# Kernel tuning notes

Hardware: AMD Instinct MI355X
Metric: run time of the kernel (lower is better)

Reference implementation:

```python
import jax, jax.numpy as jnp
import numpy as np


def squash(s, axis=-1):
    sq = jnp.sum(jnp.square(s), axis=axis, keepdims=True)
    scale = sq / (1.0 + sq) / (jnp.sqrt(sq) + 1e-08)
    return scale * s


def setup_inputs() -> dict:
    key = jax.random.key(0)
    k1, k2 = jax.random.split(key)
    # [B, input_num_caps, input_dim_caps]
    x = jax.random.normal(k1, (64, 1152, 8), dtype=jnp.float32)
    # W: [input_num_caps, num_capsules, input_dim_caps, dim_capsules]
    W = jax.random.normal(k2, (1152, 32, 8, 16), dtype=jnp.float32) * 0.05
    return {"x": x, "W": W}


def reference(x, W):
    # Original tiles x along the output-capsule axis before the einsum
    # 'bicd,icde->bice'; since the tiled copies are identical along c,
    # this is exactly 'bid,icde->bice' without materializing the tile.
    u_hat = jnp.einsum('bid,icde->bice', x, W)  # [B, I, C, E]
    b = jnp.zeros(u_hat.shape[:3], dtype=u_hat.dtype)  # [B, I, C]
    routings = 3
    v = None
    for i in range(routings):
        c = jax.nn.softmax(b, axis=-1)                 # over output capsules
        s = jnp.einsum('bic,bice->bce', c, u_hat)      # weighted sum over I
        v = squash(s)                                  # [B, C, E]
        if i < routings - 1:
            b = b + jnp.einsum('bice,bce->bic', u_hat, v)  # agreement
    return v
```

## Files before the change

### kernel.cpp

```cpp
#include <hip/hip_runtime.h>
#include <hip/hip_fp16.h>

#define B_ 64
#define I_ 1152
#define C_ 32
#define E_ 16
#define D_ 8
#define BC_ 8
#define ICt 12
#define NIC (I_/ICt)
#define ICX (NIC/8)
#define SCE (B_*C_*E_)
#define SCE2 (SCE/2)
#define WIB 8192

__device__ __forceinline__ void gload_lds16(const void* g, void* l) {
  typedef __attribute__((address_space(1))) const void GV;
  typedef __attribute__((address_space(3))) void LV;
  __builtin_amdgcn_global_load_lds((GV*)g, (LV*)l, 16, 0, 0);
}

#define WAITVM4() do { asm volatile("s_waitcnt vmcnt(4)" ::: "memory"); \
                       __builtin_amdgcn_sched_barrier(0); } while (0)
#define WAITVM2() do { asm volatile("s_waitcnt vmcnt(2)" ::: "memory"); \
                       __builtin_amdgcn_sched_barrier(0); } while (0)
#define WAITVM0() do { asm volatile("s_waitcnt vmcnt(0)" ::: "memory"); \
                       __builtin_amdgcn_sched_barrier(0); } while (0)
#define WAITLG0() do { asm volatile("s_waitcnt lgkmcnt(0)" ::: "memory"); \
                       __builtin_amdgcn_sched_barrier(0); } while (0)

typedef _Float16 h2v __attribute__((ext_vector_type(2)));

__device__ __forceinline__ float dot2f(__half2 a, __half2 b, float c) {
#if defined(__has_builtin)
#if __has_builtin(__builtin_amdgcn_fdot2)
  return __builtin_amdgcn_fdot2(__builtin_bit_cast(h2v, a),
                                __builtin_bit_cast(h2v, b), c, false);
#else
  float2 fa = __half22float2(a), fb = __half22float2(b);
  return fmaf(fa.x, fb.x, fmaf(fa.y, fb.y, c));
#endif
#else
  float2 fa = __half22float2(a), fb = __half22float2(b);
  return fmaf(fa.x, fb.x, fmaf(fa.y, fb.y, c));
#endif
}

__global__ __launch_bounds__(256)
void convert_wx(const float* __restrict__ W, const float* __restrict__ x,
                __half* __restrict__ Wh, __half2* __restrict__ xh)
{
  const int bid = blockIdx.x;
  const int t   = threadIdx.x;
  if (bid < 2304) {
    int G = bid*256 + t;
    const float4* src = (const float4*)(W + (size_t)G*8);
    float4 a = src[0], b = src[1];
    __half2 h0 = __float22half2_rn({a.x, a.y});
    __half2 h1 = __float22half2_rn({a.z, a.w});
    __half2 h2 = __float22half2_rn({b.x, b.y});
    __half2 h3 = __float22half2_rn({b.z, b.w});
    float4 o;
    o.x = __builtin_bit_cast(float, h0); o.y = __builtin_bit_cast(float, h1);
    o.z = __builtin_bit_cast(float, h2); o.w = __builtin_bit_cast(float, h3);
    *(float4*)(Wh + (size_t)G*8) = o;
  } else {
    int k = (bid - 2304)*256 + t;
    const float4* src = (const float4*)(x + (size_t)k*4);
    float4 a = src[0];
    float4 o;
    o.x = __builtin_bit_cast(float, __float22half2_rn({a.x, a.x}));
    o.y = __builtin_bit_cast(float, __float22half2_rn({a.y, a.y}));
    o.z = __builtin_bit_cast(float, __float22half2_rn({a.z, a.z}));
    o.w = __builtin_bit_cast(float, __float22half2_rn({a.w, a.w}));
    *(float4*)(xh + (size_t)k*4) = o;
  }
}

template<bool ROUTE>
__global__ __launch_bounds__(256)
void caps_pass(const __half2* __restrict__ xh, const char* __restrict__ Wh,
               const float* __restrict__ vacc, __half* __restrict__ partial)
{
  __shared__ float4 Wl[3][512];
  __shared__ __half2 xl[BC_*ICt*D_];

  const int t   = threadIdx.x;
  const int c   = t & 31;
  const int eh  = (t >> 5) & 1;
  const int bq  = t >> 6;
  const int xcd = blockIdx.x & 7;
  const int sl  = blockIdx.x >> 3;
  const int ic  = xcd * ICX + (sl >> 3);
  const int b0  = (sl & 7) * BC_;
  const int i0  = ic * ICt;

  int fsrc[2];
#pragma unroll
  for (int k = 0; k < 2; ++k) {
    int g = t + 256*k, cc = g >> 4, q = g & 15;
    fsrc[k] = cc*256 + ((q ^ (cc & 15)) << 4);
  }

  __half2 vrp[2][4];
  if (ROUTE) {
#pragma unroll
    for (int j = 0; j < 2; ++j) {
      const float4* vp = (const float4*)(vacc + (((size_t)(b0 + bq*2 + j)*C_ + c)*E_ + eh*8));
      float4 a = vp[0], b = vp[1];
      vrp[j][0] = __float22half2_rn({a.x, a.y});
      vrp[j][1] = __float22half2_rn({a.z, a.w});
      vrp[j][2] = __float22half2_rn({b.x, b.y});
      vrp[j][3] = __float22half2_rn({b.z, b.w});
    }
  }

  if (t < BC_*ICt*D_/4) {
    int b = t / 24, r = t % 24;
    float4 v = ((const float4*)(xh + ((size_t)(b0 + b)*I_ + i0)*D_))[r];
    ((float4*)xl)[b*24 + r] = v;
  }

  const char* wg = Wh + (size_t)i0 * WIB;
#pragma unroll
  for (int k = 0; k < 2; ++k) gload_lds16(wg + fsrc[k],        (char*)&Wl[0][0] + (t + 256*k)*16);
#pragma unroll
  for (int k = 0; k < 2; ++k) gload_lds16(wg + WIB + fsrc[k],  (char*)&Wl[1][0] + (t + 256*k)*16);

  __half2 accp[2][4];
#pragma unroll
  for (int j = 0; j < 2; ++j)
#pragma unroll
    for (int q = 0; q < 4; ++q) accp[j][q] = __half2{__half(0.f), __half(0.f)};

  int cur = 0;
  for (int ii = 0; ii < ICt; ++ii) {
    WAITLG0();
    __builtin_amdgcn_s_barrier();
    __builtin_amdgcn_sched_barrier(0);

    if (ii + 2 < ICt) {
      int pre = cur + 2; if (pre >= 3) pre -= 3;
      const char* wn = wg + (size_t)(ii + 2) * WIB;
#pragma unroll
      for (int k = 0; k < 2; ++k)
        gload_lds16(wn + fsrc[k], (char*)&Wl[pre][0] + (t + 256*k)*16);
    }

    if (ii < ICt - 2)       WAITVM4();
    else if (ii == ICt - 2) WAITVM2();
    else                    WAITVM0();
    __builtin_amdgcn_s_barrier();
    __builtin_amdgcn_sched_barrier(0);

    __half2 uhp[2][4];
#pragma unroll
    for (int j = 0; j < 2; ++j)
#pragma unroll
      for (int q = 0; q < 4; ++q) uhp[j][q] = __half2{__half(0.f), __half(0.f)};

    const char* wrow = (const char*)&Wl[cur][0] + c*256;
    const __half2* xr0 = xl + (bq*2 + 0)*(ICt*D_) + ii*D_;
    const __half2* xr1 = xl + (bq*2 + 1)*(ICt*D_) + ii*D_;
#pragma unroll
    for (int d = 0; d < D_; ++d) {
      float4 w4 = *(const float4*)(wrow + ((((d*2 + eh) ^ (c & 15))) << 4));
      __half2 w0 = __builtin_bit_cast(__half2, w4.x);
      __half2 w1 = __builtin_bit_cast(__half2, w4.y);
      __half2 w2 = __builtin_bit_cast(__half2, w4.z);
      __half2 w3 = __builtin_bit_cast(__half2, w4.w);
      __half2 x0 = xr0[d], x1 = xr1[d];
      uhp[0][0] = __hfma2(x0, w0, uhp[0][0]);
      uhp[0][1] = __hfma2(x0, w1, uhp[0][1]);
      uhp[0][2] = __hfma2(x0, w2, uhp[0][2]);
      uhp[0][3] = __hfma2(x0, w3, uhp[0][3]);
      uhp[1][0] = __hfma2(x1, w0, uhp[1][0]);
      uhp[1][1] = __hfma2(x1, w1, uhp[1][1]);
      uhp[1][2] = __hfma2(x1, w2, uhp[1][2]);
      uhp[1][3] = __hfma2(x1, w3, uhp[1][3]);
    }

    float coef[2];
    if (ROUTE) {
#pragma unroll
      for (int j = 0; j < 2; ++j) {
        float lg = 0.f;
#pragma unroll
        for (int q = 0; q < 4; ++q) lg = dot2f(uhp[j][q], vrp[j][q], lg);
        lg += __shfl_xor(lg, 32, 64);
        float p = __expf(lg);
        float s = p;
#pragma unroll
        for (int mk = 16; mk >= 1; mk >>= 1) s += __shfl_xor(s, mk, 64);
        coef[j] = p * __builtin_amdgcn_rcpf(s);
      }
    } else {
#pragma unroll
      for (int j = 0; j < 2; ++j) coef[j] = (1.0f / C_);
    }

#pragma unroll
    for (int j = 0; j < 2; ++j) {
      __half2 cp = __float2half2_rn(coef[j]);
#pragma unroll
      for (int q = 0; q < 4; ++q) accp[j][q] = __hfma2(cp, uhp[j][q], accp[j][q]);
    }

    cur = (cur + 1 == 3) ? 0 : cur + 1;
  }

#pragma unroll
  for (int j = 0; j < 2; ++j) {
    size_t base = ((size_t)ic * B_ + (b0 + bq*2 + j)) * (C_*E_) + (size_t)c*E_ + eh*8;
    float4 o;
    o.x = __builtin_bit_cast(float, accp[j][0]);
    o.y = __builtin_bit_cast(float, accp[j][1]);
    o.z = __builtin_bit_cast(float, accp[j][2]);
    o.w = __builtin_bit_cast(float, accp[j][3]);
    *(float4*)(partial + base) = o;
  }
}

__global__ __launch_bounds__(256)
void reduce_squash(const __half2* __restrict__ partial, float* __restrict__ vacc,
                   float* __restrict__ out, int mode)
{
  __shared__ float2 sm[256];
  const int t    = threadIdx.x;
  const int pair = blockIdx.x*64 + (t & 63);
  const int part = t >> 6;
  const __half2* p = partial + (size_t)(part*(NIC/4)) * SCE2 + pair;
  float2 s = {0.f, 0.f};
#pragma unroll 6
  for (int k = 0; k < NIC/4; ++k) {
    float2 f = __half22float2(p[(size_t)k * SCE2]);
    s.x += f.x; s.y += f.y;
  }
  sm[t] = s;
  __syncthreads();
  if (t < 64) {
    float2 a = sm[t], b = sm[t+64], c2 = sm[t+128], d = sm[t+192];
    float2 tot = {a.x+b.x+c2.x+d.x, a.y+b.y+c2.y+d.y};
    float sq = tot.x*tot.x + tot.y*tot.y;
    sq += __shfl_xor(sq, 1); sq += __shfl_xor(sq, 2); sq += __shfl_xor(sq, 4);
    float scale = sq / (1.f + sq) / (sqrtf(sq) + 1e-8f);
    float vx = scale * tot.x, vy = scale * tot.y;
    const int cell = pair * 2;
    if (mode == 0)      { vacc[cell] = vx;  vacc[cell+1] = vy;  }
    else if (mode == 1) { vacc[cell] += vx; vacc[cell+1] += vy; }
    else                { out[cell]  = vx;  out[cell+1]  = vy;  }
  }
}

extern "C" void kernel_launch(void* const* d_in, const int* in_sizes, int n_in,
                              void* d_out, int out_size, void* d_ws, size_t ws_size,
                              hipStream_t stream)
{
  const float* x = (const float*)d_in[0];
  const float* W = (const float*)d_in[1];
  float* out     = (float*)d_out;

  char* ws = (char*)d_ws;
  __half*  partial = (__half*)ws;                    ws += (size_t)NIC*SCE*2;
  float*   vacc    = (float*)ws;                     ws += (size_t)SCE*4;
  __half*  Wh      = (__half*)ws;                    ws += (size_t)I_*C_*D_*E_*2;
  __half2* xh      = (__half2*)ws;

  dim3 pg(NIC * (B_/BC_));
  const int rg = SCE2 / 64;

  convert_wx<<<2880, 256, 0, stream>>>(W, x, Wh, xh);

  caps_pass<false><<<pg, 256, 0, stream>>>(xh, (const char*)Wh, nullptr, partial);
  reduce_squash<<<rg, 256, 0, stream>>>((const __half2*)partial, vacc, nullptr, 0);
  caps_pass<true ><<<pg, 256, 0, stream>>>(xh, (const char*)Wh, vacc, partial);
  reduce_squash<<<rg, 256, 0, stream>>>((const __half2*)partial, vacc, nullptr, 1);
  caps_pass<true ><<<pg, 256, 0, stream>>>(xh, (const char*)Wh, vacc, partial);
  reduce_squash<<<rg, 256, 0, stream>>>((const __half2*)partial, vacc, out, 2);
}
```

Baseline: 73.87 us.

## Stage two input capsules per pipeline step and widen reduce parallelism

The caps_pass W pipeline now loads two input capsules' weights per stage (double-sized LDS buffers), halving the number of barrier and wait rounds per block. x values are loaded as float4 vectors into registers. reduce_squash splits the partial-sum reduction across 8 parts of 32 pairs instead of 4 parts of 64, doubling the block count. Larger LDS use (about 48KB) may reduce occupancy.

```diff
diff --git a/kernel.cpp b/kernel.cpp
--- a/kernel.cpp
+++ b/kernel.cpp
@@ -20,9 +20,9 @@
   __builtin_amdgcn_global_load_lds((GV*)g, (LV*)l, 16, 0, 0);
 }
 
+#define WAITVM8() do { asm volatile("s_waitcnt vmcnt(8)" ::: "memory"); \
+                       __builtin_amdgcn_sched_barrier(0); } while (0)
 #define WAITVM4() do { asm volatile("s_waitcnt vmcnt(4)" ::: "memory"); \
-                       __builtin_amdgcn_sched_barrier(0); } while (0)
-#define WAITVM2() do { asm volatile("s_waitcnt vmcnt(2)" ::: "memory"); \
                        __builtin_amdgcn_sched_barrier(0); } while (0)
 #define WAITVM0() do { asm volatile("s_waitcnt vmcnt(0)" ::: "memory"); \
                        __builtin_amdgcn_sched_barrier(0); } while (0)
@@ -82,7 +82,7 @@
 void caps_pass(const __half2* __restrict__ xh, const char* __restrict__ Wh,
                const float* __restrict__ vacc, __half* __restrict__ partial)
 {
-  __shared__ float4 Wl[3][512];
+  __shared__ float4 Wl[3][1024];
   __shared__ __half2 xl[BC_*ICt*D_];
 
   const int t   = threadIdx.x;
@@ -123,9 +123,11 @@
 
   const char* wg = Wh + (size_t)i0 * WIB;
 #pragma unroll
-  for (int k = 0; k < 2; ++k) gload_lds16(wg + fsrc[k],        (char*)&Wl[0][0] + (t + 256*k)*16);
-#pragma unroll
-  for (int k = 0; k < 2; ++k) gload_lds16(wg + WIB + fsrc[k],  (char*)&Wl[1][0] + (t + 256*k)*16);
+  for (int k = 0; k < 4; ++k)
+    gload_lds16(wg + (k>>1)*WIB + fsrc[k&1], (char*)&Wl[0][0] + (t + 256*k)*16);
+#pragma unroll
+  for (int k = 0; k < 4; ++k)
+    gload_lds16(wg + WIB*2 + (k>>1)*WIB + fsrc[k&1], (char*)&Wl[1][0] + (t + 256*k)*16);
 
   __half2 accp[2][4];
 #pragma unroll
@@ -134,76 +136,95 @@
     for (int q = 0; q < 4; ++q) accp[j][q] = __half2{__half(0.f), __half(0.f)};
 
   int cur = 0;
-  for (int ii = 0; ii < ICt; ++ii) {
+  for (int p = 0; p < ICt/2; ++p) {
     WAITLG0();
     __builtin_amdgcn_s_barrier();
     __builtin_amdgcn_sched_barrier(0);
 
-    if (ii + 2 < ICt) {
+    if (p + 2 < ICt/2) {
       int pre = cur + 2; if (pre >= 3) pre -= 3;
-      const char* wn = wg + (size_t)(ii + 2) * WIB;
-#pragma unroll
-      for (int k = 0; k < 2; ++k)
-        gload_lds16(wn + fsrc[k], (char*)&Wl[pre][0] + (t + 256*k)*16);
+      const char* wn = wg + (size_t)(p + 2) * (2*WIB);
+#pragma unroll
+      for (int k = 0; k < 4; ++k)
+        gload_lds16(wn + (k>>1)*WIB + fsrc[k&1], (char*)&Wl[pre][0] + (t + 256*k)*16);
     }
 
-    if (ii < ICt - 2)       WAITVM4();
-    else if (ii == ICt - 2) WAITVM2();
-    else                    WAITVM0();
+    if (p < ICt/2 - 2)       WAITVM8();
+    else if (p == ICt/2 - 2) WAITVM4();
+    else                     WAITVM0();
     __builtin_amdgcn_s_barrier();
     __builtin_amdgcn_sched_barrier(0);
 
-    __half2 uhp[2][4];
-#pragma unroll
-    for (int j = 0; j < 2; ++j)
-#pragma unroll
-      for (int q = 0; q < 4; ++q) uhp[j][q] = __half2{__half(0.f), __half(0.f)};
-
-    const char* wrow = (const char*)&Wl[cur][0] + c*256;
-    const __half2* xr0 = xl + (bq*2 + 0)*(ICt*D_) + ii*D_;
-    const __half2* xr1 = xl + (bq*2 + 1)*(ICt*D_) + ii*D_;
-#pragma unroll
-    for (int d = 0; d < D_; ++d) {
-      float4 w4 = *(const float4*)(wrow + ((((d*2 + eh) ^ (c & 15))) << 4));
-      __half2 w0 = __builtin_bit_cast(__half2, w4.x);
-      __half2 w1 = __builtin_bit_cast(__half2, w4.y);
-      __half2 w2 = __builtin_bit_cast(__half2, w4.z);
-      __half2 w3 = __builtin_bit_cast(__half2, w4.w);
-      __half2 x0 = xr0[d], x1 = xr1[d];
-      uhp[0][0] = __hfma2(x0, w0, uhp[0][0]);
-      uhp[0][1] = __hfma2(x0, w1, uhp[0][1]);
-      uhp[0][2] = __hfma2(x0, w2, uhp[0][2]);
-      uhp[0][3] = __hfma2(x0, w3, uhp[0][3]);
-      uhp[1][0] = __hfma2(x1, w0, uhp[1][0]);
-      uhp[1][1] = __hfma2(x1, w1, uhp[1][1]);
-      uhp[1][2] = __hfma2(x1, w2, uhp[1][2]);
-      uhp[1][3] = __hfma2(x1, w3, uhp[1][3]);
-    }
-
-    float coef[2];
-    if (ROUTE) {
+#pragma unroll
+    for (int il = 0; il < 2; ++il) {
+      const int ii = p*2 + il;
+
+      __half2 xd0[8], xd1[8];
+      {
+        const float4* xr = (const float4*)xl;
+        float4 a0 = xr[((bq*2 + 0)*ICt + ii)*2 + 0];
+        float4 b0v = xr[((bq*2 + 0)*ICt + ii)*2 + 1];
+        float4 a1 = xr[((bq*2 + 1)*ICt + ii)*2 + 0];
+        float4 b1v = xr[((bq*2 + 1)*ICt + ii)*2 + 1];
+        xd0[0]=__builtin_bit_cast(__half2,a0.x); xd0[1]=__builtin_bit_cast(__half2,a0.y);
+        xd0[2]=__builtin_bit_cast(__half2,a0.z); xd0[3]=__builtin_bit_cast(__half2,a0.w);
+        xd0[4]=__builtin_bit_cast(__half2,b0v.x); xd0[5]=__builtin_bit_cast(__half2,b0v.y);
+        xd0[6]=__builtin_bit_cast(__half2,b0v.z); xd0[7]=__builtin_bit_cast(__half2,b0v.w);
+        xd1[0]=__builtin_bit_cast(__half2,a1.x); xd1[1]=__builtin_bit_cast(__half2,a1.y);
+        xd1[2]=__builtin_bit_cast(__half2,a1.z); xd1[3]=__builtin_bit_cast(__half2,a1.w);
+        xd1[4]=__builtin_bit_cast(__half2,b1v.x); xd1[5]=__builtin_bit_cast(__half2,b1v.y);
+        xd1[6]=__builtin_bit_cast(__half2,b1v.z); xd1[7]=__builtin_bit_cast(__half2,b1v.w);
+      }
+
+      __half2 uhp[2][4];
+#pragma unroll
+      for (int j = 0; j < 2; ++j)
+#pragma unroll
+        for (int q = 0; q < 4; ++q) uhp[j][q] = __half2{__half(0.f), __half(0.f)};
+
+      const char* wrow = (const char*)&Wl[cur][0] + il*WIB + c*256;
+#pragma unroll
+      for (int d = 0; d < D_; ++d) {
+        float4 w4 = *(const float4*)(wrow + ((((d*2 + eh) ^ (c & 15))) << 4));
+        __half2 w0 = __builtin_bit_cast(__half2, w4.x);
+        __half2 w1 = __builtin_bit_cast(__half2, w4.y);
+        __half2 w2 = __builtin_bit_cast(__half2, w4.z);
+        __half2 w3 = __builtin_bit_cast(__half2, w4.w);
+        uhp[0][0] = __hfma2(xd0[d], w0, uhp[0][0]);
+        uhp[0][1] = __hfma2(xd0[d], w1, uhp[0][1]);
+        uhp[0][2] = __hfma2(xd0[d], w2, uhp[0][2]);
+        uhp[0][3] = __hfma2(xd0[d], w3, uhp[0][3]);
+        uhp[1][0] = __hfma2(xd1[d], w0, uhp[1][0]);
+        uhp[1][1] = __hfma2(xd1[d], w1, uhp[1][1]);
+        uhp[1][2] = __hfma2(xd1[d], w2, uhp[1][2]);
+        uhp[1][3] = __hfma2(xd1[d], w3, uhp[1][3]);
+      }
+
+      float coef[2];
+      if (ROUTE) {
+#pragma unroll
+        for (int j = 0; j < 2; ++j) {
+          float lg = 0.f;
+#pragma unroll
+          for (int q = 0; q < 4; ++q) lg = dot2f(uhp[j][q], vrp[j][q], lg);
+          lg += __shfl_xor(lg, 32, 64);
+          float pexp = __expf(lg);
+          float s = pexp;
+#pragma unroll
+          for (int mk = 16; mk >= 1; mk >>= 1) s += __shfl_xor(s, mk, 64);
+          coef[j] = pexp * __builtin_amdgcn_rcpf(s);
+        }
+      } else {
+#pragma unroll
+        for (int j = 0; j < 2; ++j) coef[j] = (1.0f / C_);
+      }
+
 #pragma unroll
       for (int j = 0; j < 2; ++j) {
-        float lg = 0.f;
-#pragma unroll
-        for (int q = 0; q < 4; ++q) lg = dot2f(uhp[j][q], vrp[j][q], lg);
-        lg += __shfl_xor(lg, 32, 64);
-        float p = __expf(lg);
-        float s = p;
-#pragma unroll
-        for (int mk = 16; mk >= 1; mk >>= 1) s += __shfl_xor(s, mk, 64);
-        coef[j] = p * __builtin_amdgcn_rcpf(s);
+        __half2 cp = __float2half2_rn(coef[j]);
+#pragma unroll
+        for (int q = 0; q < 4; ++q) accp[j][q] = __hfma2(cp, uhp[j][q], accp[j][q]);
       }
-    } else {
-#pragma unroll
-      for (int j = 0; j < 2; ++j) coef[j] = (1.0f / C_);
-    }
-
-#pragma unroll
-    for (int j = 0; j < 2; ++j) {
-      __half2 cp = __float2half2_rn(coef[j]);
-#pragma unroll
-      for (int q = 0; q < 4; ++q) accp[j][q] = __hfma2(cp, uhp[j][q], accp[j][q]);
     }
 
     cur = (cur + 1 == 3) ? 0 : cur + 1;
@@ -227,20 +248,24 @@
 {
   __shared__ float2 sm[256];
   const int t    = threadIdx.x;
-  const int pair = blockIdx.x*64 + (t & 63);
-  const int part = t >> 6;
-  const __half2* p = partial + (size_t)(part*(NIC/4)) * SCE2 + pair;
+  const int pair = blockIdx.x*32 + (t & 31);
+  const int part = t >> 5;
+  const __half2* p = partial + (size_t)(part*(NIC/8)) * SCE2 + pair;
   float2 s = {0.f, 0.f};
-#pragma unroll 6
-  for (int k = 0; k < NIC/4; ++k) {
+#pragma unroll
+  for (int k = 0; k < NIC/8; ++k) {
     float2 f = __half22float2(p[(size_t)k * SCE2]);
     s.x += f.x; s.y += f.y;
   }
   sm[t] = s;
   __syncthreads();
-  if (t < 64) {
-    float2 a = sm[t], b = sm[t+64], c2 = sm[t+128], d = sm[t+192];
-    float2 tot = {a.x+b.x+c2.x+d.x, a.y+b.y+c2.y+d.y};
+  if (t < 32) {
+    float2 tot = {0.f, 0.f};
+#pragma unroll
+    for (int pp = 0; pp < 8; ++pp) {
+      float2 v = sm[t + 32*pp];
+      tot.x += v.x; tot.y += v.y;
+    }
     float sq = tot.x*tot.x + tot.y*tot.y;
     sq += __shfl_xor(sq, 1); sq += __shfl_xor(sq, 2); sq += __shfl_xor(sq, 4);
     float scale = sq / (1.f + sq) / (sqrtf(sq) + 1e-8f);
@@ -267,7 +292,7 @@
   __half2* xh      = (__half2*)ws;
 
   dim3 pg(NIC * (B_/BC_));
-  const int rg = SCE2 / 64;
+  const int rg = SCE2 / 32;
 
   convert_wx<<<2880, 256, 0, stream>>>(W, x, Wh, xh);
 
```

Result: no change. 73.55 us (-0.4%).
